# Performance work log

Hardware: AMD Instinct MI355X
Metric: run time of the kernel (lower is better)

## Reference

```python
import jax, jax.numpy as jnp
import numpy as np

D_MODEL = 1024
NUM_HEADS = 16
D_FF = 4096
EPS = 1e-6


def _layernorm(x, alpha, beta):
    # custom LN: alpha * (x - mean) / (std + eps) + beta, std is UNBIASED (ddof=1)
    mu = jnp.mean(x, axis=-1, keepdims=True)
    var = jnp.sum((x - mu) ** 2, axis=-1, keepdims=True) / (x.shape[-1] - 1)
    return alpha * (x - mu) / (jnp.sqrt(var) + EPS) + beta


def setup_inputs() -> dict:
    key = jax.random.key(0)
    ks = jax.random.split(key, 8)
    B, S, D, F = 1, 4096, D_MODEL, D_FF
    s = 0.02
    inp = {
        "x": jax.random.normal(ks[0], (B, S, D), dtype=jnp.float32),
        "Wq": jax.random.normal(ks[1], (D, D), dtype=jnp.float32) * s,
        "bq": jnp.zeros((D,), jnp.float32),
        "Wk": jax.random.normal(ks[2], (D, D), dtype=jnp.float32) * s,
        "bk": jnp.zeros((D,), jnp.float32),
        "Wv": jax.random.normal(ks[3], (D, D), dtype=jnp.float32) * s,
        "bv": jnp.zeros((D,), jnp.float32),
        "Wo": jax.random.normal(ks[4], (D, D), dtype=jnp.float32) * s,
        "bo": jnp.zeros((D,), jnp.float32),
        "ln1_a": jnp.ones((1,), jnp.float32),
        "ln1_b": jnp.zeros((1,), jnp.float32),
        "W1": jax.random.normal(ks[5], (D, F), dtype=jnp.float32) * s,
        "b1": jnp.zeros((F,), jnp.float32),
        "W2": jax.random.normal(ks[6], (F, D), dtype=jnp.float32) * s,
        "b2": jnp.zeros((D,), jnp.float32),
        "ln2_a": jnp.ones((1,), jnp.float32),
        "ln2_b": jnp.zeros((1,), jnp.float32),
    }
    return inp


def reference(x, Wq, bq, Wk, bk, Wv, bv, Wo, bo, ln1_a, ln1_b,
              W1, b1, W2, b2, ln2_a, ln2_b):
    B, S, D = x.shape
    H = NUM_HEADS
    dk = D // H

    # --- residual 1: pre-LN self-attention ---
    h = _layernorm(x, ln1_a, ln1_b)
    Q = (h @ Wq + bq).reshape(B, S, H, dk)
    K = (h @ Wk + bk).reshape(B, S, H, dk)
    V = (h @ Wv + bv).reshape(B, S, H, dk)
    scores = jnp.einsum("bqhd,bkhd->bhqk", Q, K) / jnp.sqrt(jnp.float32(dk))
    attn = jax.nn.softmax(scores, axis=-1)  # [B,H,S,S] materialized as in source
    ctx = jnp.einsum("bhqk,bkhd->bqhd", attn, V).reshape(B, S, D)
    x = x + (ctx @ Wo + bo)  # dropout=0 -> identity

    # --- residual 2: pre-LN feed-forward ---
    h2 = _layernorm(x, ln2_a, ln2_b)
    ffn = jax.nn.relu(h2 @ W1 + b1) @ W2 + b2
    return x + ffn
```

## Files before the change

kernel.cpp:

```cpp
#include <hip/hip_runtime.h>
#include <hip/hip_bf16.h>

typedef __attribute__((ext_vector_type(8))) __bf16 bf16x8;
typedef __attribute__((ext_vector_type(4))) __bf16 bf16x4;
typedef __attribute__((ext_vector_type(4))) float f32x4;
typedef __attribute__((ext_vector_type(4))) short sh4;
typedef __attribute__((ext_vector_type(8))) short sh8;

#define MFMA(a, b, c) __builtin_amdgcn_mfma_f32_16x16x32_bf16(a, b, c, 0, 0, 0)

#if defined(__has_builtin)
#if __has_builtin(__builtin_amdgcn_mfma_f32_16x16x16bf16_1k)
#define HAVE_MFMA16 1
#endif
#endif

__device__ __forceinline__ f32x4 mfma_pv(sh4 a, sh4 b, f32x4 c) {
#ifdef HAVE_MFMA16
    return __builtin_amdgcn_mfma_f32_16x16x16bf16_1k(a, b, c, 0, 0, 0);
#else
    sh8 aw = {a[0], a[1], a[2], a[3], 0, 0, 0, 0};
    sh8 bw = {b[0], b[1], b[2], b[3], 0, 0, 0, 0};
    return MFMA(__builtin_bit_cast(bf16x8, aw), __builtin_bit_cast(bf16x8, bw), c);
#endif
}

__device__ __forceinline__ sh4 pk4(float a, float b, float c, float d) {
    __hip_bfloat162 lo = __float22bfloat162_rn(float2{a, b});
    __hip_bfloat162 hi = __float22bfloat162_rn(float2{c, d});
    union { struct { __hip_bfloat162 lo, hi; } p; sh4 s; } u;
    u.p.lo = lo; u.p.hi = hi;
    return u.s;
}

__global__ void detect_k(const void* wq, float* flag) {
    int lane = threadIdx.x;
    const __bf16* p = (const __bf16*)wq;
    float mx = 0.f;
    for (int i = lane; i < 1024; i += 64) {
        float v = (float)p[i];
        if (v != v) mx = 2.f;
        v = fabsf(v);
        if (v > mx) mx = v;
    }
    for (int o = 1; o < 64; o <<= 1) {
        float t = __shfl_xor(mx, o);
        if (t > mx) mx = t;
    }
    if (lane == 0) *flag = (mx > 1.0f) ? 1.f : 0.f;
}

__device__ __forceinline__ float ldany(const void* p, size_t i, bool f32) {
    return f32 ? ((const float*)p)[i] : (float)(((const __bf16*)p)[i]);
}

__global__ void cvt_small_k(const void* bq, const void* bk, const void* bv, const void* bo,
                            const void* b1, const void* b2,
                            const void* l1a, const void* l1b, const void* l2a, const void* l2b,
                            __bf16* dst, const float* flag) {
    bool f32 = *flag > 0.5f;
    const void* srcs[10] = {bq, bk, bv, bo, b1, b2, l1a, l1b, l2a, l2b};
    const int offs[10] = {1024, 2048, 3072, 4096, 5120, 9216, 10240, 10241, 10242, 10243};
    const int ns[10]   = {1024, 1024, 1024, 1024, 4096, 1024, 1, 1, 1, 1};
    for (int t = 0; t < 10; ++t)
        for (int j = threadIdx.x; j < ns[t]; j += blockDim.x)
            dst[offs[t] + j] = (__bf16)ldany(srcs[t], j, f32);
}

__device__ __forceinline__ void tr_body(const void* in, __bf16* out, int R, int C, bool f32,
                                        int bx, int by, int x, int y) {
    __shared__ __bf16 t[32][33];
    for (int i = 0; i < 32; i += 8)
        t[y + i][x] = (__bf16)ldany(in, (size_t)(by + y + i) * C + bx + x, f32);
    __syncthreads();
    for (int i = 0; i < 32; i += 8)
        out[(size_t)(bx + y + i) * R + by + x] = t[x][y + i];
}

__global__ void transpose_cvt(const void* in, __bf16* out, int R, int C, const float* flag) {
    tr_body(in, out, R, C, *flag > 0.5f, blockIdx.x * 32, blockIdx.y * 32,
            threadIdx.x, threadIdx.y);
}

__global__ void transpose4_cvt(const void* i0, const void* i1, const void* i2, const void* i3,
                               __bf16* o0, __bf16* o1, __bf16* o2, __bf16* o3,
                               const float* flag) {
    const void* in = blockIdx.z == 0 ? i0 : blockIdx.z == 1 ? i1 : blockIdx.z == 2 ? i2 : i3;
    __bf16* out = blockIdx.z == 0 ? o0 : blockIdx.z == 1 ? o1 : blockIdx.z == 2 ? o2 : o3;
    tr_body(in, out, 1024, 1024, *flag > 0.5f, blockIdx.x * 32, blockIdx.y * 32,
            threadIdx.x, threadIdx.y);
}

__global__ __launch_bounds__(256) void layernorm_k(const void* x, int xmode, const float* flag,
                                                   __bf16* out,
                                                   const __bf16* alpha, const __bf16* beta) {
    int row = blockIdx.x * 4 + (threadIdx.x >> 6);
    int lane = threadIdx.x & 63;
    bool f32 = xmode && (*flag > 0.5f);
    float v[16];
    if (f32) {
        const float4* xr = (const float4*)((const float*)x + (size_t)row * 1024 + lane * 16);
#pragma unroll
        for (int q = 0; q < 4; ++q) {
            float4 r = xr[q];
            v[q * 4 + 0] = r.x; v[q * 4 + 1] = r.y; v[q * 4 + 2] = r.z; v[q * 4 + 3] = r.w;
        }
    } else {
        const __bf16* xr = (const __bf16*)x + (size_t)row * 1024 + lane * 16;
        bf16x8 h0 = *(const bf16x8*)xr;
        bf16x8 h1 = *(const bf16x8*)(xr + 8);
#pragma unroll
        for (int i = 0; i < 8; ++i) { v[i] = (float)h0[i]; v[8 + i] = (float)h1[i]; }
    }
    float s = 0.f, ss = 0.f;
#pragma unroll
    for (int i = 0; i < 16; ++i) { s += v[i]; ss += v[i] * v[i]; }
#pragma unroll
    for (int o = 1; o < 64; o <<= 1) { s += __shfl_xor(s, o); ss += __shfl_xor(ss, o); }
    float mu = s * (1.f / 1024.f);
    float var = (ss - 1024.f * mu * mu) * (1.f / 1023.f);
    float inv = 1.f / (sqrtf(var) + 1e-6f);
    float al = (float)alpha[0], be = (float)beta[0];
    bf16x8 o0, o1;
#pragma unroll
    for (int i = 0; i < 8; ++i) {
        o0[i] = (__bf16)((v[i] - mu) * inv * al + be);
        o1[i] = (__bf16)((v[8 + i] - mu) * inv * al + be);
    }
    __bf16* orow = out + (size_t)row * 1024;
    *(bf16x8*)(orow + lane * 16) = o0;
    *(bf16x8*)(orow + lane * 16 + 8) = o1;
}

__device__ __forceinline__ void swz_store(__bf16* buf, int hh, int ktt, int rr2, int cc2,
                                          float v) {
    size_t off = (((size_t)hh * 64 + ktt) << 12) + rr2 * 64 +
                 (((cc2 >> 3) ^ (rr2 & 7)) << 3) + (cc2 & 7);
    buf[off] = (__bf16)v;
}

__global__ __launch_bounds__(256) void gemm_bt(const __bf16* __restrict__ A, int lda,
                                               const __bf16* __restrict__ Bt, int ldb,
                                               const __bf16* __restrict__ bias_n,
                                               const __bf16* __restrict__ bias_m,
                                               const void* res, int res_mode,
                                               const float* flag,
                                               void* C, int out_pf,
                                               int M, int N, int K, int relu,
                                               __bf16* swzbuf, int swz) {
    __shared__ __bf16 As[128 * 32];
    __shared__ __bf16 Bs[128 * 32];
    const int tid = threadIdx.x;
    const int m0 = blockIdx.y * 128;
    const int n0 = blockIdx.x * 128;
    const int w = tid >> 6, lane = tid & 63;
    const int wr = (w >> 1) * 64, wc = (w & 1) * 64;
    const int lm = lane & 15, lg = lane >> 4;
    const bool f32 = *flag > 0.5f;
    const bool rf32 = (res_mode == 2) && f32;
    const bool of32 = out_pf && f32;

    f32x4 acc[4][4] = {};
    for (int k0 = 0; k0 < K; k0 += 32) {
#pragma unroll
        for (int i = 0; i < 2; ++i) {
            int c = i * 256 + tid;
            int row = c >> 2, kk = (c & 3) * 8;
            __builtin_amdgcn_global_load_lds(
                (const __attribute__((address_space(1))) void*)(A + (size_t)(m0 + row) * lda + k0 + kk),
                (__attribute__((address_space(3))) void*)(As + c * 8), 16, 0, 0);
            __builtin_amdgcn_global_load_lds(
                (const __attribute__((address_space(1))) void*)(Bt + (size_t)(n0 + row) * ldb + k0 + kk),
                (__attribute__((address_space(3))) void*)(Bs + c * 8), 16, 0, 0);
        }
        __syncthreads();
        bf16x8 a[4], b[4];
#pragma unroll
        for (int t = 0; t < 4; ++t)
            a[t] = *(const bf16x8*)(As + (wr + t * 16 + lm) * 32 + lg * 8);
#pragma unroll
        for (int t = 0; t < 4; ++t)
            b[t] = *(const bf16x8*)(Bs + (wc + t * 16 + lm) * 32 + lg * 8);
#pragma unroll
        for (int mt = 0; mt < 4; ++mt)
#pragma unroll
            for (int nt = 0; nt < 4; ++nt)
                acc[mt][nt] = MFMA(a[mt], b[nt], acc[mt][nt]);
        __syncthreads();
    }
#pragma unroll
    for (int mt = 0; mt < 4; ++mt) {
#pragma unroll
        for (int nt = 0; nt < 4; ++nt) {
            int col = n0 + wc + nt * 16 + lm;
            float bn = bias_n ? (float)bias_n[col] : 0.f;
#pragma unroll
            for (int r = 0; r < 4; ++r) {
                int row = m0 + wr + mt * 16 + lg * 4 + r;
                float vv = acc[mt][nt][r] + bn;
                if (bias_m) vv += (float)bias_m[row];
                if (relu) vv = fmaxf(vv, 0.f);
                if (swz == 1 && col >= 1024) {
                    swz_store(swzbuf, (col - 1024) >> 6, row >> 6, row & 63, (col - 1024) & 63, vv);
                } else if (swz == 2) {
                    swz_store(swzbuf, row >> 6, col >> 6, row & 63, col & 63, vv);
                } else {
                    size_t idx = (size_t)row * N + col;
                    if (res_mode) vv += rf32 ? ((const float*)res)[idx]
                                             : (float)(((const __bf16*)res)[idx]);
                    if (of32) ((float*)C)[idx] = vv;
                    else ((__bf16*)C)[idx] = (__bf16)vv;
                }
            }
        }
    }
}

__global__ __launch_bounds__(256) void gemm_n64(const __bf16* __restrict__ A, int lda,
                                                const __bf16* __restrict__ Bt, int ldb,
                                                const __bf16* __restrict__ bias_n,
                                                const __bf16* __restrict__ bias_m,
                                                const void* res, int res_mode,
                                                const float* flag,
                                                void* C, int out_pf,
                                                int M, int N, int K, int relu,
                                                __bf16* swzbuf, int swz) {
    __shared__ __bf16 As[128 * 32];
    __shared__ __bf16 Bs[64 * 32];
    const int tid = threadIdx.x;
    const int m0 = blockIdx.y * 128;
    const int n0 = blockIdx.x * 64;
    const int w = tid >> 6, lane = tid & 63;
    const int wr = (w >> 1) * 64, wc = (w & 1) * 32;
    const int lm = lane & 15, lg = lane >> 4;
    const bool f32 = *flag > 0.5f;
    const bool rf32 = (res_mode == 2) && f32;
    const bool of32 = out_pf && f32;

    f32x4 acc[4][2] = {};
    for (int k0 = 0; k0 < K; k0 += 32) {
#pragma unroll
        for (int i = 0; i < 2; ++i) {
            int c = i * 256 + tid;
            int row = c >> 2, kk = (c & 3) * 8;
            __builtin_amdgcn_global_load_lds(
                (const __attribute__((address_space(1))) void*)(A + (size_t)(m0 + row) * lda + k0 + kk),
                (__attribute__((address_space(3))) void*)(As + c * 8), 16, 0, 0);
        }
        {
            int row = tid >> 2, kk = (tid & 3) * 8;
            __builtin_amdgcn_global_load_lds(
                (const __attribute__((address_space(1))) void*)(Bt + (size_t)(n0 + row) * ldb + k0 + kk),
                (__attribute__((address_space(3))) void*)(Bs + tid * 8), 16, 0, 0);
        }
        __syncthreads();
        bf16x8 a[4], b[2];
#pragma unroll
        for (int t = 0; t < 4; ++t)
            a[t] = *(const bf16x8*)(As + (wr + t * 16 + lm) * 32 + lg * 8);
#pragma unroll
        for (int t = 0; t < 2; ++t)
            b[t] = *(const bf16x8*)(Bs + (wc + t * 16 + lm) * 32 + lg * 8);
#pragma unroll
        for (int mt = 0; mt < 4; ++mt)
#pragma unroll
            for (int nt = 0; nt < 2; ++nt)
                acc[mt][nt] = MFMA(a[mt], b[nt], acc[mt][nt]);
        __syncthreads();
    }
#pragma unroll
    for (int mt = 0; mt < 4; ++mt) {
#pragma unroll
        for (int nt = 0; nt < 2; ++nt) {
            int col = n0 + wc + nt * 16 + lm;
            float bn = bias_n ? (float)bias_n[col] : 0.f;
#pragma unroll
            for (int r = 0; r < 4; ++r) {
                int row = m0 + wr + mt * 16 + lg * 4 + r;
                float vv = acc[mt][nt][r] + bn;
                if (bias_m) vv += (float)bias_m[row];
                if (relu) vv = fmaxf(vv, 0.f);
                if (swz == 2) {
                    swz_store(swzbuf, row >> 6, col >> 6, row & 63, col & 63, vv);
                } else {
                    size_t idx = (size_t)row * N + col;
                    if (res_mode) vv += rf32 ? ((const float*)res)[idx]
                                             : (float)(((const __bf16*)res)[idx]);
                    if (of32) ((float*)C)[idx] = vv;
                    else ((__bf16*)C)[idx] = (__bf16)vv;
                }
            }
        }
    }
}

__global__ __launch_bounds__(256) void attn_ks2(const __bf16* __restrict__ Q, int ldq,
                                                const __bf16* __restrict__ Kswz,
                                                const __bf16* __restrict__ Vswz,
                                                __bf16* __restrict__ Opart,
                                                float* __restrict__ lpart) {
    constexpr int S = 4096;
    __shared__ __bf16 lds[2 * 8192];
    const int h = blockIdx.y, z = blockIdx.z;
    const int q0 = blockIdx.x * 128;
    const int tid = threadIdx.x, w = tid >> 6, lane = tid & 63;
    const int lm = lane & 15, lg = lane >> 4;

    const __bf16* gK = Kswz + (((size_t)h * 64 + z * 32) << 12);
    const __bf16* gV = Vswz + (((size_t)h * 64 + z * 32) << 12);

    bf16x8 qf[2][2];
#pragma unroll
    for (int qc = 0; qc < 2; ++qc) {
        const __bf16* qp = Q + (size_t)(q0 + w * 32 + qc * 16 + lm) * ldq + h * 64;
        qf[qc][0] = *(const bf16x8*)(qp + lg * 8);
        qf[qc][1] = *(const bf16x8*)(qp + 32 + lg * 8);
#pragma unroll
        for (int hh = 0; hh < 2; ++hh) {
            bf16x8 t = qf[qc][hh];
#pragma unroll
            for (int i = 0; i < 8; ++i) t[i] = (__bf16)((float)t[i] * 0.1803368801f);
            qf[qc][hh] = t;
        }
    }
    const bf16x4 ones_h = {(__bf16)1.f, (__bf16)1.f, (__bf16)1.f, (__bf16)1.f};
    const sh4 ones = __builtin_bit_cast(sh4, ones_h);

    f32x4 o_[4][2] = {};
    f32x4 l_[2] = {};

    auto issue = [&](int t) {
        __bf16* dK = lds + (t & 1) * 8192;
        __bf16* dV = dK + 4096;
        const __bf16* sK = gK + ((size_t)t << 12);
        const __bf16* sV = gV + ((size_t)t << 12);
#pragma unroll
        for (int i = 0; i < 2; ++i) {
            int c = i * 256 + tid;
            __builtin_amdgcn_global_load_lds(
                (const __attribute__((address_space(1))) void*)(sK + c * 8),
                (__attribute__((address_space(3))) void*)(dK + c * 8), 16, 0, 0);
            __builtin_amdgcn_global_load_lds(
                (const __attribute__((address_space(1))) void*)(sV + c * 8),
                (__attribute__((address_space(3))) void*)(dV + c * 8), 16, 0, 0);
        }
    };
    issue(0);
    for (int t = 0; t < 32; ++t) {
        __syncthreads();
        if (t < 31) issue(t + 1);
        const __bf16* Kt = lds + (t & 1) * 8192;
        const __bf16* Vt = Kt + 4096;

        sh4 pb[4][2];
#pragma unroll
        for (int mt = 0; mt < 4; ++mt) {
            int rr = mt * 16 + lm;
            const __bf16* kr = Kt + rr * 64;
            bf16x8 kf0 = *(const bf16x8*)(kr + ((lg ^ (rr & 7)) << 3));
            bf16x8 kf1 = *(const bf16x8*)(kr + (((4 + lg) ^ (rr & 7)) << 3));
#pragma unroll
            for (int qc = 0; qc < 2; ++qc) {
                f32x4 s = (f32x4){0.f, 0.f, 0.f, 0.f};
                s = MFMA(kf0, qf[qc][0], s);
                s = MFMA(kf1, qf[qc][1], s);
                pb[mt][qc] = pk4(exp2f(s[0]), exp2f(s[1]), exp2f(s[2]), exp2f(s[3]));
            }
        }
#pragma unroll
        for (int mtd = 0; mtd < 4; ++mtd) {
            int rr = mtd * 16 + lm;
            const __bf16* vr = Vt + rr * 64;
#pragma unroll
            for (int ck = 0; ck < 4; ++ck) {
                int chunk = (ck * 2 + (lg >> 1)) ^ (rr & 7);
                sh4 va = *(const sh4*)(vr + chunk * 8 + (lg & 1) * 4);
                o_[mtd][0] = mfma_pv(va, pb[ck][0], o_[mtd][0]);
                o_[mtd][1] = mfma_pv(va, pb[ck][1], o_[mtd][1]);
            }
        }
#pragma unroll
        for (int ck = 0; ck < 4; ++ck) {
            l_[0] = mfma_pv(ones, pb[ck][0], l_[0]);
            l_[1] = mfma_pv(ones, pb[ck][1], l_[1]);
        }
    }

    __syncthreads();
#pragma unroll
    for (int qc = 0; qc < 2; ++qc) {
#pragma unroll
        for (int mtd = 0; mtd < 4; ++mtd) {
            sh4 ov = pk4(o_[mtd][qc][0], o_[mtd][qc][1], o_[mtd][qc][2], o_[mtd][qc][3]);
            *(sh4*)(lds + (w * 32 + qc * 16 + lm) * 72 + mtd * 16 + lg * 4) = ov;
        }
        if (lg == 0)
            lpart[(size_t)(h * 2 + z) * S + q0 + w * 32 + qc * 16 + lm] = l_[qc][0];
    }
    __syncthreads();
    __bf16* Ob = Opart + (((size_t)(h * 2 + z) * S + q0) << 6);
    int row = tid >> 1, co = (tid & 1) * 32;
#pragma unroll
    for (int b = 0; b < 4; ++b)
        *(uint4*)(Ob + row * 64 + co + b * 8) = *(const uint4*)(lds + row * 72 + co + b * 8);
}

__global__ __launch_bounds__(256) void attn_comb(const __bf16* __restrict__ Opart,
                                                 const float* __restrict__ lpart,
                                                 __bf16* __restrict__ ctx) {
    constexpr int S = 4096;
#pragma unroll
    for (int it = 0; it < 4; ++it) {
        int task = blockIdx.x * 1024 + it * 256 + threadIdx.x;
        int q = task >> 7, c8 = task & 127, h = c8 >> 3, d8 = (c8 & 7) * 8;
        const __bf16* p0 = Opart + (((size_t)(h * 2 + 0) * S + q) << 6) + d8;
        const __bf16* p1 = Opart + (((size_t)(h * 2 + 1) * S + q) << 6) + d8;
        float inv = 1.f / (lpart[(size_t)(h * 2 + 0) * S + q] + lpart[(size_t)(h * 2 + 1) * S + q]);
        bf16x8 a = *(const bf16x8*)p0, b = *(const bf16x8*)p1, o;
#pragma unroll
        for (int i = 0; i < 8; ++i) o[i] = (__bf16)(((float)a[i] + (float)b[i]) * inv);
        *(bf16x8*)(ctx + (size_t)q * 1024 + c8 * 8) = o;
    }
}

__global__ __launch_bounds__(256) void attn_v3(const __bf16* __restrict__ Q, int ldq,
                                               const __bf16* __restrict__ Kg, int ldk,
                                               const __bf16* __restrict__ VT,
                                               __bf16* __restrict__ ctx) {
    constexpr int S = 4096, D = 1024, LDT = 72;
    __shared__ __bf16 lds[128 * LDT];
    __bf16* Kt = lds;
    __bf16* Vt = lds + 64 * LDT;
    const int h = blockIdx.y;
    const int q0 = blockIdx.x * 128;
    const int tid = threadIdx.x, w = tid >> 6, lane = tid & 63;
    const int lm = lane & 15, lg = lane >> 4;
    bf16x8 qf[2][2];
#pragma unroll
    for (int qc = 0; qc < 2; ++qc) {
        const __bf16* qp = Q + (size_t)(q0 + w * 32 + qc * 16 + lm) * ldq + h * 64;
        qf[qc][0] = *(const bf16x8*)(qp + lg * 8);
        qf[qc][1] = *(const bf16x8*)(qp + 32 + lg * 8);
#pragma unroll
        for (int hh = 0; hh < 2; ++hh) {
            bf16x8 t = qf[qc][hh];
#pragma unroll
            for (int i = 0; i < 8; ++i) t[i] = (__bf16)((float)t[i] * 0.1803368801f);
            qf[qc][hh] = t;
        }
    }
    const bf16x4 ones_h = {(__bf16)1.f, (__bf16)1.f, (__bf16)1.f, (__bf16)1.f};
    const sh4 ones = __builtin_bit_cast(sh4, ones_h);
    f32x4 o_[4][2] = {};
    f32x4 l_[2] = {};
    for (int kt = 0; kt < S / 64; ++kt) {
        __syncthreads();
#pragma unroll
        for (int i = 0; i < 2; ++i) {
            int c = i * 256 + tid;
            int rr = c >> 3, cc = (c & 7) * 8;
            *(uint4*)(Kt + rr * LDT + cc) =
                *(const uint4*)(Kg + (size_t)(kt * 64 + rr) * ldk + h * 64 + cc);
            *(uint4*)(Vt + rr * LDT + cc) =
                *(const uint4*)(VT + (size_t)(h * 64 + rr) * S + kt * 64 + cc);
        }
        __syncthreads();
        sh4 pb[4][2];
#pragma unroll
        for (int mt = 0; mt < 4; ++mt) {
            bf16x8 kf0 = *(const bf16x8*)(Kt + (mt * 16 + lm) * LDT + lg * 8);
            bf16x8 kf1 = *(const bf16x8*)(Kt + (mt * 16 + lm) * LDT + 32 + lg * 8);
#pragma unroll
            for (int qc = 0; qc < 2; ++qc) {
                f32x4 s = (f32x4){0.f, 0.f, 0.f, 0.f};
                s = MFMA(kf0, qf[qc][0], s);
                s = MFMA(kf1, qf[qc][1], s);
                pb[mt][qc] = pk4(exp2f(s[0]), exp2f(s[1]), exp2f(s[2]), exp2f(s[3]));
            }
        }
#pragma unroll
        for (int mtd = 0; mtd < 4; ++mtd)
#pragma unroll
            for (int ck = 0; ck < 4; ++ck) {
                sh4 va = *(const sh4*)(Vt + (mtd * 16 + lm) * LDT + ck * 16 + lg * 4);
                o_[mtd][0] = mfma_pv(va, pb[ck][0], o_[mtd][0]);
                o_[mtd][1] = mfma_pv(va, pb[ck][1], o_[mtd][1]);
            }
#pragma unroll
        for (int ck = 0; ck < 4; ++ck) {
            l_[0] = mfma_pv(ones, pb[ck][0], l_[0]);
            l_[1] = mfma_pv(ones, pb[ck][1], l_[1]);
        }
    }
    __syncthreads();
    float inv[2] = {1.f / l_[0][0], 1.f / l_[1][0]};
#pragma unroll
    for (int qc = 0; qc < 2; ++qc)
#pragma unroll
        for (int mtd = 0; mtd < 4; ++mtd)
#pragma unroll
            for (int r = 0; r < 4; ++r)
                lds[(w * 32 + qc * 16 + lm) * LDT + mtd * 16 + lg * 4 + r] =
                    (__bf16)(o_[mtd][qc][r] * inv[qc]);
    __syncthreads();
    int row = tid >> 1, cb = (tid & 1) * 32;
#pragma unroll
    for (int b = 0; b < 4; ++b)
        *(uint4*)(ctx + (size_t)(q0 + row) * D + h * 64 + cb + b * 8) =
            *(const uint4*)(lds + row * LDT + cb + b * 8);
}

extern "C" void kernel_launch(void* const* d_in, const int* in_sizes, int n_in,
                              void* d_out, int out_size, void* d_ws, size_t ws_size,
                              hipStream_t stream) {
    const void* x    = d_in[0];
    const void* Wq   = d_in[1];
    const void* bq   = d_in[2];
    const void* Wk   = d_in[3];
    const void* bk   = d_in[4];
    const void* Wv   = d_in[5];
    const void* bv   = d_in[6];
    const void* Wo   = d_in[7];
    const void* bo   = d_in[8];
    const void* ln1a = d_in[9];
    const void* ln1b = d_in[10];
    const void* W1   = d_in[11];
    const void* b1   = d_in[12];
    const void* W2   = d_in[13];
    const void* b2   = d_in[14];
    const void* ln2a = d_in[15];
    const void* ln2b = d_in[16];

    constexpr size_t M1 = 1u << 20;
    __bf16* ws = (__bf16*)d_ws;
    float* flagF = (float*)ws;
    __bf16* bmir = ws;
    dim3 tb(32, 8);
    const bool big = ws_size >= (size_t)(32.25 * 2 * M1) + 4096;

    detect_k<<<1, 64, 0, stream>>>(Wq, flagF);
    cvt_small_k<<<1, 256, 0, stream>>>(bq, bk, bv, bo, b1, b2, ln1a, ln1b, ln2a, ln2b,
                                       bmir, flagF);

    if (big) {
        __bf16* WqT = ws + M1 / 4;
        __bf16* WkT = WqT + M1;
        __bf16* WvT = ws + 2 * M1 + M1 / 4;
        __bf16* WoT = ws + 3 * M1 + M1 / 4;
        __bf16* W2T = ws + M1 / 4;
        float* lpart = (float*)(ws + M1 / 4);
        __bf16* hb  = ws + 4 * M1 + M1 / 4;
        __bf16* h2  = hb;
        __bf16* QKb = ws + 8 * M1 + M1 / 4;
        __bf16* x2  = QKb;
        __bf16* W1T = ws + 12 * M1 + M1 / 4;
        __bf16* Kswz = ws + 16 * M1 + M1 / 4;
        __bf16* ctx  = Kswz;
        __bf16* Vswz = ws + 20 * M1 + M1 / 4;
        __bf16* Opart = ws + 24 * M1 + M1 / 4;
        __bf16* f1  = ws + 16 * M1 + M1 / 4;

        transpose4_cvt<<<dim3(32, 32, 4), tb, 0, stream>>>(Wq, Wk, Wv, Wo,
                                                           WqT, WkT, WvT, WoT, flagF);
        layernorm_k<<<1024, 256, 0, stream>>>(x, 1, flagF, hb, bmir + 10240, bmir + 10241);
        gemm_bt<<<dim3(16, 32), 256, 0, stream>>>(hb, 1024, WqT, 1024, bmir + 1024, nullptr,
                                                  nullptr, 0, flagF, QKb, 0, 4096, 2048, 1024, 0,
                                                  Kswz, 1);
        gemm_n64<<<dim3(64, 8), 256, 0, stream>>>(WvT, 1024, hb, 1024, nullptr, bmir + 3072,
                                                  nullptr, 0, flagF, nullptr, 0, 1024, 4096, 1024, 0,
                                                  Vswz, 2);
        attn_ks2<<<dim3(32, 16, 2), 256, 0, stream>>>(QKb, 2048, Kswz, Vswz, Opart, lpart);
        attn_comb<<<512, 256, 0, stream>>>(Opart, lpart, ctx);
        transpose_cvt<<<dim3(128, 32), tb, 0, stream>>>(W1, W1T, 1024, 4096, flagF);
        gemm_n64<<<dim3(16, 32), 256, 0, stream>>>(ctx, 1024, WoT, 1024, bmir + 4096, nullptr,
                                                   x, 2, flagF, x2, 0, 4096, 1024, 1024, 0,
                                                   nullptr, 0);
        transpose_cvt<<<dim3(32, 128), tb, 0, stream>>>(W2, W2T, 4096, 1024, flagF);
        layernorm_k<<<1024, 256, 0, stream>>>(x2, 0, flagF, h2, bmir + 10242, bmir + 10243);
        gemm_bt<<<dim3(32, 32), 256, 0, stream>>>(h2, 1024, W1T, 1024, bmir + 5120, nullptr,
                                                  nullptr, 0, flagF, f1, 0, 4096, 4096, 1024, 1,
                                                  nullptr, 0);
        gemm_n64<<<dim3(16, 32), 256, 0, stream>>>(f1, 4096, W2T, 4096, bmir + 9216, nullptr,
                                                   x2, 1, flagF, d_out, 1, 4096, 1024, 4096, 0,
                                                   nullptr, 0);
    } else {
        constexpr size_t Qn = 1u << 18;
        __bf16* WqT = ws + Qn;
        __bf16* WoT = WqT;
        __bf16* WkT = ws + 5 * Qn;
        __bf16* WvT = ws + 9 * Qn;
        __bf16* hb  = ws + 13 * Qn;
        __bf16* f1q = hb;
        __bf16* ctx = ws + 29 * Qn;
        __bf16* W2T = ctx;
        __bf16* QKb = ws + 45 * Qn;
        __bf16* x2  = QKb;
        __bf16* Kb  = ws + 61 * Qn;
        __bf16* h2  = Kb;
        __bf16* VTb = ws + 77 * Qn;
        __bf16* W1T = VTb;
        transpose_cvt<<<dim3(32, 32), tb, 0, stream>>>(Wq, WqT, 1024, 1024, flagF);
        transpose_cvt<<<dim3(32, 32), tb, 0, stream>>>(Wk, WkT, 1024, 1024, flagF);
        transpose_cvt<<<dim3(32, 32), tb, 0, stream>>>(Wv, WvT, 1024, 1024, flagF);
        layernorm_k<<<1024, 256, 0, stream>>>(x, 1, flagF, hb, bmir + 10240, bmir + 10241);
        gemm_bt<<<dim3(8, 32), 256, 0, stream>>>(hb, 1024, WqT, 1024, bmir + 1024, nullptr,
                                                 nullptr, 0, flagF, QKb, 0, 4096, 1024, 1024, 0,
                                                 nullptr, 0);
        gemm_bt<<<dim3(8, 32), 256, 0, stream>>>(hb, 1024, WkT, 1024, bmir + 2048, nullptr,
                                                 nullptr, 0, flagF, Kb, 0, 4096, 1024, 1024, 0,
                                                 nullptr, 0);
        gemm_n64<<<dim3(64, 8), 256, 0, stream>>>(WvT, 1024, hb, 1024, nullptr, bmir + 3072,
                                                  nullptr, 0, flagF, VTb, 0, 1024, 4096, 1024, 0,
                                                  nullptr, 0);
        attn_v3<<<dim3(32, 16), 256, 0, stream>>>(QKb, 1024, Kb, 1024, VTb, ctx);
        transpose_cvt<<<dim3(32, 32), tb, 0, stream>>>(Wo, WoT, 1024, 1024, flagF);
        gemm_n64<<<dim3(16, 32), 256, 0, stream>>>(ctx, 1024, WoT, 1024, bmir + 4096, nullptr,
                                                   x, 2, flagF, x2, 0, 4096, 1024, 1024, 0,
                                                   nullptr, 0);
        layernorm_k<<<1024, 256, 0, stream>>>(x2, 0, flagF, h2, bmir + 10242, bmir + 10243);
        transpose_cvt<<<dim3(128, 32), tb, 0, stream>>>(W1, W1T, 1024, 4096, flagF);
        transpose_cvt<<<dim3(32, 128), tb, 0, stream>>>(W2, W2T, 4096, 1024, flagF);
        for (int ck = 0; ck < 2; ++ck) {
            gemm_bt<<<dim3(16, 32), 256, 0, stream>>>(h2, 1024, W1T + (size_t)ck * 2048 * 1024,
                                                      1024, bmir + 5120 + ck * 2048, nullptr,
                                                      nullptr, 0, flagF, f1q, 0, 4096, 2048, 1024, 1,
                                                      nullptr, 0);
            gemm_n64<<<dim3(16, 32), 256, 0, stream>>>(f1q, 2048, W2T + ck * 2048, 4096,
                                                       ck == 0 ? bmir + 9216 : nullptr, nullptr,
                                                       x2, 1, flagF, ck == 1 ? d_out : (void*)x2,
                                                       ck == 1 ? 1 : 0, 4096, 1024, 2048, 0,
                                                       nullptr, 0);
        }
    }
}
```

Measured before the change: 537.9 us.

## Use K=32 MFMA for PV, BK=64 swizzled GEMM tiles, fuse prep kernels

The attention PV and row-sum products now pack two 16-wide probability chunks into one 8-element operand and issue the 16x16x32 MFMA instead of 16x16x16. This halves the number of MFMA instructions for those products. The n64 GEMM moves from a K step of 32 to 64 and XOR-swizzles its LDS layout to avoid bank conflicts, which halves the number of barriers per K. The detect and bias-convert kernels are merged into one launch, and exp2 uses the hardware builtin, at the cost of more LDS per GEMM block.

```diff
diff --git a/kernel.cpp b/kernel.cpp
--- a/kernel.cpp
+++ b/kernel.cpp
@@ -2,28 +2,19 @@
 #include <hip/hip_bf16.h>
 
 typedef __attribute__((ext_vector_type(8))) __bf16 bf16x8;
-typedef __attribute__((ext_vector_type(4))) __bf16 bf16x4;
 typedef __attribute__((ext_vector_type(4))) float f32x4;
 typedef __attribute__((ext_vector_type(4))) short sh4;
 typedef __attribute__((ext_vector_type(8))) short sh8;
 
 #define MFMA(a, b, c) __builtin_amdgcn_mfma_f32_16x16x32_bf16(a, b, c, 0, 0, 0)
 
-#if defined(__has_builtin)
-#if __has_builtin(__builtin_amdgcn_mfma_f32_16x16x16bf16_1k)
-#define HAVE_MFMA16 1
+#if __has_builtin(__builtin_amdgcn_exp2f)
+#define EXP2(x) __builtin_amdgcn_exp2f(x)
+#else
+#define EXP2(x) exp2f(x)
 #endif
-#endif
-
-__device__ __forceinline__ f32x4 mfma_pv(sh4 a, sh4 b, f32x4 c) {
-#ifdef HAVE_MFMA16
-    return __builtin_amdgcn_mfma_f32_16x16x16bf16_1k(a, b, c, 0, 0, 0);
-#else
-    sh8 aw = {a[0], a[1], a[2], a[3], 0, 0, 0, 0};
-    sh8 bw = {b[0], b[1], b[2], b[3], 0, 0, 0, 0};
-    return MFMA(__builtin_bit_cast(bf16x8, aw), __builtin_bit_cast(bf16x8, bw), c);
-#endif
-}
+
+union P8 { struct { sh4 lo, hi; } p; sh8 v; };
 
 __device__ __forceinline__ sh4 pk4(float a, float b, float c, float d) {
     __hip_bfloat162 lo = __float22bfloat162_rn(float2{a, b});
@@ -33,37 +24,40 @@
     return u.s;
 }
 
-__global__ void detect_k(const void* wq, float* flag) {
-    int lane = threadIdx.x;
+__device__ __forceinline__ float ldany(const void* p, size_t i, bool f32) {
+    return f32 ? ((const float*)p)[i] : (float)(((const __bf16*)p)[i]);
+}
+
+__global__ void prep_k(const void* wq, float* flag,
+                       const void* bq, const void* bk, const void* bv, const void* bo,
+                       const void* b1, const void* b2,
+                       const void* l1a, const void* l1b, const void* l2a, const void* l2b,
+                       __bf16* dst) {
+    __shared__ float red[256];
+    __shared__ float fls;
+    int tid = threadIdx.x;
     const __bf16* p = (const __bf16*)wq;
     float mx = 0.f;
-    for (int i = lane; i < 1024; i += 64) {
+    for (int i = tid; i < 1024; i += 256) {
         float v = (float)p[i];
         if (v != v) mx = 2.f;
         v = fabsf(v);
         if (v > mx) mx = v;
     }
-    for (int o = 1; o < 64; o <<= 1) {
-        float t = __shfl_xor(mx, o);
-        if (t > mx) mx = t;
-    }
-    if (lane == 0) *flag = (mx > 1.0f) ? 1.f : 0.f;
-}
-
-__device__ __forceinline__ float ldany(const void* p, size_t i, bool f32) {
-    return f32 ? ((const float*)p)[i] : (float)(((const __bf16*)p)[i]);
-}
-
-__global__ void cvt_small_k(const void* bq, const void* bk, const void* bv, const void* bo,
-                            const void* b1, const void* b2,
-                            const void* l1a, const void* l1b, const void* l2a, const void* l2b,
-                            __bf16* dst, const float* flag) {
-    bool f32 = *flag > 0.5f;
+    red[tid] = mx;
+    __syncthreads();
+    for (int s = 128; s > 0; s >>= 1) {
+        if (tid < s) red[tid] = fmaxf(red[tid], red[tid + s]);
+        __syncthreads();
+    }
+    if (tid == 0) { fls = (red[0] > 1.0f) ? 1.f : 0.f; *flag = fls; }
+    __syncthreads();
+    bool f32 = fls > 0.5f;
     const void* srcs[10] = {bq, bk, bv, bo, b1, b2, l1a, l1b, l2a, l2b};
     const int offs[10] = {1024, 2048, 3072, 4096, 5120, 9216, 10240, 10241, 10242, 10243};
     const int ns[10]   = {1024, 1024, 1024, 1024, 4096, 1024, 1, 1, 1, 1};
     for (int t = 0; t < 10; ++t)
-        for (int j = threadIdx.x; j < ns[t]; j += blockDim.x)
+        for (int j = tid; j < ns[t]; j += blockDim.x)
             dst[offs[t] + j] = (__bf16)ldany(srcs[t], j, f32);
 }
 
@@ -225,47 +219,56 @@
                                                 void* C, int out_pf,
                                                 int M, int N, int K, int relu,
                                                 __bf16* swzbuf, int swz) {
-    __shared__ __bf16 As[128 * 32];
-    __shared__ __bf16 Bs[64 * 32];
+    __shared__ __bf16 As[128 * 64];
+    __shared__ __bf16 Bs[64 * 64];
     const int tid = threadIdx.x;
     const int m0 = blockIdx.y * 128;
     const int n0 = blockIdx.x * 64;
     const int w = tid >> 6, lane = tid & 63;
     const int wr = (w >> 1) * 64, wc = (w & 1) * 32;
     const int lm = lane & 15, lg = lane >> 4;
+    const int sw = lm & 7;
     const bool f32 = *flag > 0.5f;
     const bool rf32 = (res_mode == 2) && f32;
     const bool of32 = out_pf && f32;
 
     f32x4 acc[4][2] = {};
-    for (int k0 = 0; k0 < K; k0 += 32) {
+    for (int k0 = 0; k0 < K; k0 += 64) {
+#pragma unroll
+        for (int i = 0; i < 4; ++i) {
+            int c = i * 256 + tid;
+            int row = c >> 3, ch = c & 7;
+            __builtin_amdgcn_global_load_lds(
+                (const __attribute__((address_space(1))) void*)(A + (size_t)(m0 + row) * lda + k0 + ((ch ^ (row & 7)) << 3)),
+                (__attribute__((address_space(3))) void*)(As + c * 8), 16, 0, 0);
+        }
 #pragma unroll
         for (int i = 0; i < 2; ++i) {
             int c = i * 256 + tid;
-            int row = c >> 2, kk = (c & 3) * 8;
+            int row = c >> 3, ch = c & 7;
             __builtin_amdgcn_global_load_lds(
-                (const __attribute__((address_space(1))) void*)(A + (size_t)(m0 + row) * lda + k0 + kk),
-                (__attribute__((address_space(3))) void*)(As + c * 8), 16, 0, 0);
-        }
-        {
-            int row = tid >> 2, kk = (tid & 3) * 8;
-            __builtin_amdgcn_global_load_lds(
-                (const __attribute__((address_space(1))) void*)(Bt + (size_t)(n0 + row) * ldb + k0 + kk),
-                (__attribute__((address_space(3))) void*)(Bs + tid * 8), 16, 0, 0);
-        }
-        __syncthreads();
-        bf16x8 a[4], b[2];
+                (const __attribute__((address_space(1))) void*)(Bt + (size_t)(n0 + row) * ldb + k0 + ((ch ^ (row & 7)) << 3)),
+                (__attribute__((address_space(3))) void*)(Bs + c * 8), 16, 0, 0);
+        }
+        __syncthreads();
+        bf16x8 a[4][2], b[2][2];
 #pragma unroll
         for (int t = 0; t < 4; ++t)
-            a[t] = *(const bf16x8*)(As + (wr + t * 16 + lm) * 32 + lg * 8);
+#pragma unroll
+            for (int h = 0; h < 2; ++h)
+                a[t][h] = *(const bf16x8*)(As + (wr + t * 16 + lm) * 64 + ((((h << 2) | lg) ^ sw) << 3));
 #pragma unroll
         for (int t = 0; t < 2; ++t)
-            b[t] = *(const bf16x8*)(Bs + (wc + t * 16 + lm) * 32 + lg * 8);
+#pragma unroll
+            for (int h = 0; h < 2; ++h)
+                b[t][h] = *(const bf16x8*)(Bs + (wc + t * 16 + lm) * 64 + ((((h << 2) | lg) ^ sw) << 3));
 #pragma unroll
         for (int mt = 0; mt < 4; ++mt)
 #pragma unroll
-            for (int nt = 0; nt < 2; ++nt)
-                acc[mt][nt] = MFMA(a[mt], b[nt], acc[mt][nt]);
+            for (int nt = 0; nt < 2; ++nt) {
+                acc[mt][nt] = MFMA(a[mt][0], b[nt][0], acc[mt][nt]);
+                acc[mt][nt] = MFMA(a[mt][1], b[nt][1], acc[mt][nt]);
+            }
         __syncthreads();
     }
 #pragma unroll
@@ -323,8 +326,9 @@
             qf[qc][hh] = t;
         }
     }
-    const bf16x4 ones_h = {(__bf16)1.f, (__bf16)1.f, (__bf16)1.f, (__bf16)1.f};
-    const sh4 ones = __builtin_bit_cast(sh4, ones_h);
+    bf16x8 ones8;
+#pragma unroll
+    for (int i = 0; i < 8; ++i) ones8[i] = (__bf16)1.f;
 
     f32x4 o_[4][2] = {};
     f32x4 l_[2] = {};
@@ -352,7 +356,7 @@
         const __bf16* Kt = lds + (t & 1) * 8192;
         const __bf16* Vt = Kt + 4096;
 
-        sh4 pb[4][2];
+        P8 pb[2][2];
 #pragma unroll
         for (int mt = 0; mt < 4; ++mt) {
             int rr = mt * 16 + lm;
@@ -364,7 +368,9 @@
                 f32x4 s = (f32x4){0.f, 0.f, 0.f, 0.f};
                 s = MFMA(kf0, qf[qc][0], s);
                 s = MFMA(kf1, qf[qc][1], s);
-                pb[mt][qc] = pk4(exp2f(s[0]), exp2f(s[1]), exp2f(s[2]), exp2f(s[3]));
+                sh4 e = pk4(EXP2(s[0]), EXP2(s[1]), EXP2(s[2]), EXP2(s[3]));
+                if (mt & 1) pb[mt >> 1][qc].p.hi = e;
+                else        pb[mt >> 1][qc].p.lo = e;
             }
         }
 #pragma unroll
@@ -372,17 +378,20 @@
             int rr = mtd * 16 + lm;
             const __bf16* vr = Vt + rr * 64;
 #pragma unroll
-            for (int ck = 0; ck < 4; ++ck) {
-                int chunk = (ck * 2 + (lg >> 1)) ^ (rr & 7);
-                sh4 va = *(const sh4*)(vr + chunk * 8 + (lg & 1) * 4);
-                o_[mtd][0] = mfma_pv(va, pb[ck][0], o_[mtd][0]);
-                o_[mtd][1] = mfma_pv(va, pb[ck][1], o_[mtd][1]);
+            for (int cp = 0; cp < 2; ++cp) {
+                int cbase = cp * 4 + (lg >> 1);
+                P8 va;
+                va.p.lo = *(const sh4*)(vr + ((cbase ^ (rr & 7)) << 3) + (lg & 1) * 4);
+                va.p.hi = *(const sh4*)(vr + (((cbase + 2) ^ (rr & 7)) << 3) + (lg & 1) * 4);
+                bf16x8 vab = __builtin_bit_cast(bf16x8, va.v);
+                o_[mtd][0] = MFMA(vab, __builtin_bit_cast(bf16x8, pb[cp][0].v), o_[mtd][0]);
+                o_[mtd][1] = MFMA(vab, __builtin_bit_cast(bf16x8, pb[cp][1].v), o_[mtd][1]);
             }
         }
 #pragma unroll
-        for (int ck = 0; ck < 4; ++ck) {
-            l_[0] = mfma_pv(ones, pb[ck][0], l_[0]);
-            l_[1] = mfma_pv(ones, pb[ck][1], l_[1]);
+        for (int cp = 0; cp < 2; ++cp) {
+            l_[0] = MFMA(ones8, __builtin_bit_cast(bf16x8, pb[cp][0].v), l_[0]);
+            l_[1] = MFMA(ones8, __builtin_bit_cast(bf16x8, pb[cp][1].v), l_[1]);
         }
     }
 
@@ -449,8 +458,9 @@
             qf[qc][hh] = t;
         }
     }
-    const bf16x4 ones_h = {(__bf16)1.f, (__bf16)1.f, (__bf16)1.f, (__bf16)1.f};
-    const sh4 ones = __builtin_bit_cast(sh4, ones_h);
+    bf16x8 ones8;
+#pragma unroll
+    for (int i = 0; i < 8; ++i) ones8[i] = (__bf16)1.f;
     f32x4 o_[4][2] = {};
     f32x4 l_[2] = {};
     for (int kt = 0; kt < S / 64; ++kt) {
@@ -465,7 +475,7 @@
                 *(const uint4*)(VT + (size_t)(h * 64 + rr) * S + kt * 64 + cc);
         }
         __syncthreads();
-        sh4 pb[4][2];
+        P8 pb[2][2];
 #pragma unroll
         for (int mt = 0; mt < 4; ++mt) {
             bf16x8 kf0 = *(const bf16x8*)(Kt + (mt * 16 + lm) * LDT + lg * 8);
@@ -475,21 +485,28 @@
                 f32x4 s = (f32x4){0.f, 0.f, 0.f, 0.f};
                 s = MFMA(kf0, qf[qc][0], s);
                 s = MFMA(kf1, qf[qc][1], s);
-                pb[mt][qc] = pk4(exp2f(s[0]), exp2f(s[1]), exp2f(s[2]), exp2f(s[3]));
+                sh4 e = pk4(EXP2(s[0]), EXP2(s[1]), EXP2(s[2]), EXP2(s[3]));
+                if (mt & 1) pb[mt >> 1][qc].p.hi = e;
+                else        pb[mt >> 1][qc].p.lo = e;
             }
         }
 #pragma unroll
-        for (int mtd = 0; mtd < 4; ++mtd)
-#pragma unroll
-            for (int ck = 0; ck < 4; ++ck) {
-                sh4 va = *(const sh4*)(Vt + (mtd * 16 + lm) * LDT + ck * 16 + lg * 4);
-                o_[mtd][0] = mfma_pv(va, pb[ck][0], o_[mtd][0]);
-                o_[mtd][1] = mfma_pv(va, pb[ck][1], o_[mtd][1]);
+        for (int mtd = 0; mtd < 4; ++mtd) {
+            const __bf16* vrow = Vt + (mtd * 16 + lm) * LDT;
+#pragma unroll
+            for (int cp = 0; cp < 2; ++cp) {
+                P8 va;
+                va.p.lo = *(const sh4*)(vrow + cp * 32 + lg * 4);
+                va.p.hi = *(const sh4*)(vrow + cp * 32 + 16 + lg * 4);
+                bf16x8 vab = __builtin_bit_cast(bf16x8, va.v);
+                o_[mtd][0] = MFMA(vab, __builtin_bit_cast(bf16x8, pb[cp][0].v), o_[mtd][0]);
+                o_[mtd][1] = MFMA(vab, __builtin_bit_cast(bf16x8, pb[cp][1].v), o_[mtd][1]);
             }
-#pragma unroll
-        for (int ck = 0; ck < 4; ++ck) {
-            l_[0] = mfma_pv(ones, pb[ck][0], l_[0]);
-            l_[1] = mfma_pv(ones, pb[ck][1], l_[1]);
+        }
+#pragma unroll
+        for (int cp = 0; cp < 2; ++cp) {
+            l_[0] = MFMA(ones8, __builtin_bit_cast(bf16x8, pb[cp][0].v), l_[0]);
+            l_[1] = MFMA(ones8, __builtin_bit_cast(bf16x8, pb[cp][1].v), l_[1]);
         }
     }
     __syncthreads();
@@ -538,9 +555,8 @@
     dim3 tb(32, 8);
     const bool big = ws_size >= (size_t)(32.25 * 2 * M1) + 4096;
 
-    detect_k<<<1, 64, 0, stream>>>(Wq, flagF);
-    cvt_small_k<<<1, 256, 0, stream>>>(bq, bk, bv, bo, b1, b2, ln1a, ln1b, ln2a, ln2b,
-                                       bmir, flagF);
+    prep_k<<<1, 256, 0, stream>>>(Wq, flagF, bq, bk, bv, bo, b1, b2,
+                                  ln1a, ln1b, ln2a, ln2b, bmir);
 
     if (big) {
         __bf16* WqT = ws + M1 / 4;
```

Measured after the change: 488.2 us. -9.2%, faster.
